# Performance work log

Measured on AMD Instinct MI355X. Metric: run time of the kernel, lower is better.

## Reference

```python
import jax, jax.numpy as jnp
import numpy as np

NEG_SLOPE = 0.2  # PyG GATConv default leaky_relu slope

def gat_conv(x, src, dst, W, a_src, a_dst, bias, N):
    # Linear transform
    h = x @ W                      # [N, D]
    # Per-node attention logits (heads=1)
    al_src = h @ a_src             # [N]
    al_dst = h @ a_dst             # [N]
    e = jax.nn.leaky_relu(al_src[src] + al_dst[dst], NEG_SLOPE)  # [E]
    # Segment softmax over incoming edges of each destination node
    m = jax.ops.segment_max(e, dst, num_segments=N)
    ex = jnp.exp(e - m[dst])
    denom = jax.ops.segment_sum(ex, dst, num_segments=N)
    alpha = ex / denom[dst]        # [E]
    # Weighted scatter-aggregate of source features
    out = jax.ops.segment_sum(h[src] * alpha[:, None], dst, num_segments=N)
    return out + bias

def setup_inputs() -> dict:
    key = jax.random.key(0)
    ks = jax.random.split(key, 10)
    N, E, F_in, H, O = 50000, 800000, 128, 64, 64
    x = jax.random.normal(ks[0], (N, F_in), dtype=jnp.float32)
    edge_index = jax.random.randint(ks[1], (2, E), 0, N, dtype=jnp.int32)
    s = lambda k, shp, fan: jax.random.normal(k, shp, dtype=jnp.float32) / np.sqrt(fan)
    return {
        'x': x, 'edge_index': edge_index,
        'W1': s(ks[2], (F_in, H), F_in), 'a_src1': s(ks[3], (H,), H), 'a_dst1': s(ks[4], (H,), H), 'b1': jnp.zeros((H,), jnp.float32),
        'W2': s(ks[5], (H, O), H), 'a_src2': s(ks[6], (O,), O), 'a_dst2': s(ks[7], (O,), O), 'b2': jnp.zeros((O,), jnp.float32),
    }

def reference(x, edge_index, W1, a_src1, a_dst1, b1, W2, a_src2, a_dst2, b2):
    N = x.shape[0]
    loops = jnp.arange(N, dtype=edge_index.dtype)  # PyG adds self-loops by default
    src = jnp.concatenate([edge_index[0], loops])
    dst = jnp.concatenate([edge_index[1], loops])
    h = gat_conv(x, src, dst, W1, a_src1, a_dst1, b1, N)
    h = jax.nn.relu(h)
    # dropout(p=0.6) is identity in eval mode
    out = gat_conv(h, src, dst, W2, a_src2, a_dst2, b2, N)
    return out
```

## Files before the change

kernel.cpp:

```cpp
#include <hip/hip_runtime.h>
#include <hip/hip_bf16.h>

#define DEV static __device__ __forceinline__

typedef short bf16x8 __attribute__((ext_vector_type(8)));
typedef float f32x4  __attribute__((ext_vector_type(4)));
typedef unsigned u32x4 __attribute__((ext_vector_type(4)));

union U4 { uint4 u; bf16x8 s; };

DEV float b2f(__hip_bfloat16 v) { return __bfloat162float(v); }
DEV float lrelu(float e) { return e > 0.f ? e : 0.2f * e; }

DEV unsigned short f2bu(float f) {
    __hip_bfloat16 b = __float2bfloat16(f);
    return *reinterpret_cast<unsigned short*>(&b);
}
DEV float bu2f(unsigned short u) { return __uint_as_float((unsigned)u << 16); }

DEV float loadF(const void* p, size_t i, int f32) {
    if (f32) return ((const float*)p)[i];
    return b2f(((const __hip_bfloat16*)p)[i]);
}

DEV uint4 pack8(const unsigned short* t) {
    uint4 v;
    v.x = (unsigned)t[0] | ((unsigned)t[1] << 16);
    v.y = (unsigned)t[2] | ((unsigned)t[3] << 16);
    v.z = (unsigned)t[4] | ((unsigned)t[5] << 16);
    v.w = (unsigned)t[6] | ((unsigned)t[7] << 16);
    return v;
}

DEV u32x4 pack8v(const unsigned short* t) {
    u32x4 v;
    v.x = (unsigned)t[0] | ((unsigned)t[1] << 16);
    v.y = (unsigned)t[2] | ((unsigned)t[3] << 16);
    v.z = (unsigned)t[4] | ((unsigned)t[5] << 16);
    v.w = (unsigned)t[6] | ((unsigned)t[7] << 16);
    return v;
}

__global__ __launch_bounds__(1024) void k_detect(
    const void* a0, int n0, const void* a1, int n1, const void* a2, int n2,
    const void* a3, int n3, const void* a4, int n4, const void* a5, int n5,
    const void* a6, int n6, const void* a7, int n7, const void* a8, int n8,
    int* __restrict__ flags)
{
    const void* ps[9] = {a0,a1,a2,a3,a4,a5,a6,a7,a8};
    const int   ns[9] = {n0,n1,n2,n3,n4,n5,n6,n7,n8};
    const int w = threadIdx.x >> 6, lane = threadIdx.x & 63;
    if (w >= 9) return;
    const unsigned short* p = (const unsigned short*)ps[w];
    const int n = ns[w];
    bool insane = false;
#pragma unroll
    for (int r = 0; r < 4; ++r) {
        int idx = lane + r * 64;
        if (idx < n) {
            unsigned short u = p[idx];
            unsigned e = (u >> 7) & 0xFFu;
            insane |= (e >= 0xC8u) || (e == 0u && (u & 0x7Fu) != 0u);
        }
    }
    unsigned long long m = __ballot(insane);
    if (lane == 0) flags[w] = (m != 0ull) ? 1 : 0;
}

DEV void edge_sd(int i, int E, const int* __restrict__ src, const int* __restrict__ dst,
                 int& s, int& d) {
    if (i < E) { s = src[i]; d = dst[i]; }
    else       { s = d = i - E; }
}

#define G_BIN 128

__global__ __launch_bounds__(256) void k_binA(
    const int* __restrict__ src, const int* __restrict__ dst,
    int* __restrict__ hist, int E, int EA, int chunk)
{
    __shared__ int cnt[256];
    const int tid = threadIdx.x;
    cnt[tid] = 0;
    __syncthreads();
    const int lo = blockIdx.x * chunk;
    const int hi = min(lo + chunk, EA);
    for (int i = lo + tid; i < hi; i += 256) {
        int s, d; edge_sd(i, E, src, dst, s, d);
        atomicAdd(&cnt[d >> 8], 1);
    }
    __syncthreads();
    hist[blockIdx.x * 256 + tid] = cnt[tid];
}

__global__ __launch_bounds__(G_BIN) void k_binB1(
    const int* __restrict__ hist, int* __restrict__ offs_rel,
    int* __restrict__ btot)
{
    __shared__ int sm[G_BIN];
    const int t = threadIdx.x;
    const int b = blockIdx.x;
    int v = hist[t * 256 + b];
    sm[t] = v;
    __syncthreads();
#pragma unroll
    for (int off = 1; off < G_BIN; off <<= 1) {
        int u = (t >= off) ? sm[t - off] : 0;
        __syncthreads();
        sm[t] += u;
        __syncthreads();
    }
    offs_rel[t * 256 + b] = sm[t] - v;
    if (t == G_BIN - 1) btot[b] = sm[t];
}

__global__ __launch_bounds__(256) void k_binB2(
    const int* __restrict__ btot, int* __restrict__ bstart)
{
    __shared__ int sm[256];
    const int tid = threadIdx.x;
    int v = btot[tid];
    sm[tid] = v;
    __syncthreads();
#pragma unroll
    for (int off = 1; off < 256; off <<= 1) {
        int t = (tid >= off) ? sm[tid - off] : 0;
        __syncthreads();
        sm[tid] += t;
        __syncthreads();
    }
    bstart[tid] = sm[tid] - v;
    if (tid == 255) bstart[256] = sm[255];
}

__global__ __launch_bounds__(256) void k_binC(
    const int* __restrict__ src, const int* __restrict__ dst,
    const int* __restrict__ offs_rel, const int* __restrict__ bstart,
    unsigned* __restrict__ ebuf, int E, int EA, int chunk)
{
    __shared__ int cur[256];
    const int tid = threadIdx.x;
    cur[tid] = bstart[tid] + offs_rel[blockIdx.x * 256 + tid];
    __syncthreads();
    const int lo = blockIdx.x * chunk;
    const int hi = min(lo + chunk, EA);
    for (int i = lo + tid; i < hi; i += 256) {
        int s, d; edge_sd(i, E, src, dst, s, d);
        int pos = atomicAdd(&cur[d >> 8], 1);
        ebuf[pos] = ((unsigned)(d & 255) << 17) | (unsigned)s;
    }
}

__global__ __launch_bounds__(256) void k_binD(
    const unsigned* __restrict__ ebuf, const int* __restrict__ bstart,
    int* __restrict__ row_ptr, int* __restrict__ col, int N)
{
    __shared__ int cnt[256];
    __shared__ int pfx[256];
    const int tid = threadIdx.x;
    const int b = blockIdx.x;
    const int lo = bstart[b], hi = bstart[b + 1];
    cnt[tid] = 0;
    __syncthreads();
    for (int i = lo + tid; i < hi; i += 256)
        atomicAdd(&cnt[ebuf[i] >> 17], 1);
    __syncthreads();
    const int c = cnt[tid];
    pfx[tid] = c;
    __syncthreads();
#pragma unroll
    for (int off = 1; off < 256; off <<= 1) {
        int t = (tid >= off) ? pfx[tid - off] : 0;
        __syncthreads();
        pfx[tid] += t;
        __syncthreads();
    }
    const int excl = pfx[tid] - c;
    const int d = b * 256 + tid;
    if (d <= N) row_ptr[d] = lo + excl;
    __syncthreads();
    cnt[tid] = lo + excl;
    __syncthreads();
    for (int i = lo + tid; i < hi; i += 256) {
        unsigned v = ebuf[i];
        int pos = atomicAdd(&cnt[v >> 17], 1);
        col[pos] = (int)(v & 0x1FFFFu);
    }
}

__global__ __launch_bounds__(256) void k_gemm1(
    const void* __restrict__ x, const void* __restrict__ W,
    const void* __restrict__ a_s, const void* __restrict__ a_d,
    const int* __restrict__ flags,
    __hip_bfloat16* __restrict__ h, float* __restrict__ als, float* __restrict__ ald,
    int N)
{
    __shared__ __align__(16) unsigned short sMem[2 * 64 * 136];
    __shared__ float sAs[64], sAd[64];
    unsigned short* sA = sMem;
    unsigned short* sB = sMem + 64 * 136;
    float* sOut = (float*)sMem;

    const int tid = threadIdx.x;
    const int row0 = blockIdx.x * 64;
    const int fx = flags[0], fw = flags[1];

    if (tid < 64) sAs[tid] = loadF(a_s, tid, flags[2]);
    else if (tid < 128) sAd[tid - 64] = loadF(a_d, tid - 64, flags[3]);

    if (!fx) {
        const uint4* xg = (const uint4*)x;
#pragma unroll
        for (int it = 0; it < 2; ++it) {
            int g = tid + it * 256;
            int r = g >> 4, c16 = g & 15;
            uint4 v = (row0 + r < N) ? xg[(size_t)(row0 + r) * 16 + c16]
                                     : make_uint4(0, 0, 0, 0);
            *(uint4*)(sA + r * 136 + c16 * 8) = v;
        }
    } else {
        for (int i = tid; i < 64 * 128; i += 256) {
            int r = i >> 7, k = i & 127;
            float v = (row0 + r < N) ? ((const float*)x)[(size_t)(row0 + r) * 128 + k] : 0.f;
            sA[r * 136 + k] = f2bu(v);
        }
    }
    if (!fw) {
        const unsigned short* Wg = (const unsigned short*)W;
        const int n = tid & 63;
        int k0 = (tid >> 6) * 8;
#pragma unroll
        for (int rep = 0; rep < 4; ++rep, k0 += 32) {
            unsigned short t[8];
#pragma unroll
            for (int j = 0; j < 8; ++j) t[j] = Wg[(size_t)(k0 + j) * 64 + n];
            *(uint4*)(sB + n * 136 + k0) = pack8(t);
        }
    } else {
        const float* Wg = (const float*)W;
        for (int i = tid; i < 128 * 64; i += 256) {
            int k = i >> 6, n = i & 63;
            sB[n * 136 + k] = f2bu(Wg[i]);
        }
    }
    __syncthreads();

    const int w = tid >> 6, lane = tid & 63;
    const int m0 = w * 16;
    const int qr = lane >> 4;
    const int lc = lane & 15;

    bf16x8 afrag[4];
#pragma unroll
    for (int c = 0; c < 4; ++c) {
        U4 u; u.u = *(const uint4*)(sA + (m0 + lc) * 136 + c * 32 + qr * 8);
        afrag[c] = u.s;
    }
    f32x4 accs[4];
#pragma unroll
    for (int nt = 0; nt < 4; ++nt) {
        f32x4 acc = {0.f, 0.f, 0.f, 0.f};
#pragma unroll
        for (int c = 0; c < 4; ++c) {
            U4 u; u.u = *(const uint4*)(sB + (nt * 16 + lc) * 136 + c * 32 + qr * 8);
            acc = __builtin_amdgcn_mfma_f32_16x16x32_bf16(afrag[c], u.s, acc, 0, 0, 0);
        }
        accs[nt] = acc;
    }
    __syncthreads();

#pragma unroll
    for (int nt = 0; nt < 4; ++nt)
#pragma unroll
        for (int reg = 0; reg < 4; ++reg)
            sOut[(m0 + qr * 4 + reg) * 68 + nt * 16 + lc] = accs[nt][reg];
    __syncthreads();

    {
        const int r = tid >> 2, seg = tid & 3;
        const int row = row0 + r;
        const float* po = sOut + r * 68 + seg * 16;
        float ps = 0.f, pd = 0.f;
        unsigned short ob[16];
#pragma unroll
        for (int i = 0; i < 16; ++i) {
            float v = po[i];
            ps = fmaf(v, sAs[seg * 16 + i], ps);
            pd = fmaf(v, sAd[seg * 16 + i], pd);
            ob[i] = f2bu(v);
        }
        if (row < N) {
            uint4* hp = (uint4*)((unsigned short*)h + (size_t)row * 64 + seg * 16);
            hp[0] = pack8(ob);
            hp[1] = pack8(ob + 8);
        }
        ps += __shfl_xor(ps, 1, 64); ps += __shfl_xor(ps, 2, 64);
        pd += __shfl_xor(pd, 1, 64); pd += __shfl_xor(pd, 2, 64);
        if (seg == 0 && row < N) { als[row] = ps; ald[row] = pd; }
    }
}

__global__ __launch_bounds__(256) void k_gemm2(
    __hip_bfloat16* __restrict__ agg, const void* __restrict__ b1,
    const void* __restrict__ W, const void* __restrict__ a_s,
    const void* __restrict__ a_d, const int* __restrict__ flags,
    float* __restrict__ als, float* __restrict__ ald, int N)
{
    __shared__ __align__(16) unsigned short sMem[2 * 64 * 72];
    __shared__ float sAs[64], sAd[64], sBias[64];
    unsigned short* sA = sMem;
    unsigned short* sB = sMem + 64 * 72;
    float* sOut = (float*)sMem;

    const int tid = threadIdx.x;
    const int row0 = blockIdx.x * 64;
    const int fw = flags[5];

    if (tid < 64) sAs[tid] = loadF(a_s, tid, flags[6]);
    else if (tid < 128) sAd[tid - 64] = loadF(a_d, tid - 64, flags[7]);
    else if (tid < 192) sBias[tid - 128] = loadF(b1, tid - 128, flags[4]);
    __syncthreads();

    {
        const uint4* ag = (const uint4*)agg;
#pragma unroll
        for (int it = 0; it < 2; ++it) {
            int g = tid + it * 256;
            int r = g >> 3, c8 = g & 7;
            uint4 v = (row0 + r < N) ? ag[(size_t)(row0 + r) * 8 + c8]
                                     : make_uint4(0, 0, 0, 0);
            unsigned short in[8] = {
                (unsigned short)(v.x & 0xFFFF), (unsigned short)(v.x >> 16),
                (unsigned short)(v.y & 0xFFFF), (unsigned short)(v.y >> 16),
                (unsigned short)(v.z & 0xFFFF), (unsigned short)(v.z >> 16),
                (unsigned short)(v.w & 0xFFFF), (unsigned short)(v.w >> 16)};
            unsigned short ob[8];
#pragma unroll
            for (int j = 0; j < 8; ++j) {
                float t = bu2f(in[j]) + sBias[c8 * 8 + j];
                ob[j] = f2bu(t > 0.f ? t : 0.f);
            }
            *(uint4*)(sA + r * 72 + c8 * 8) = pack8(ob);
        }
    }
    if (!fw) {
        const unsigned short* Wg = (const unsigned short*)W;
        const int n = tid & 63;
        int k0 = (tid >> 6) * 8;
#pragma unroll
        for (int rep = 0; rep < 2; ++rep, k0 += 32) {
            unsigned short t[8];
#pragma unroll
            for (int j = 0; j < 8; ++j) t[j] = Wg[(size_t)(k0 + j) * 64 + n];
            *(uint4*)(sB + n * 72 + k0) = pack8(t);
        }
    } else {
        const float* Wg = (const float*)W;
        for (int i = tid; i < 64 * 64; i += 256) {
            int k = i >> 6, n = i & 63;
            sB[n * 72 + k] = f2bu(Wg[i]);
        }
    }
    __syncthreads();

    const int w = tid >> 6, lane = tid & 63;
    const int m0 = w * 16;
    const int qr = lane >> 4, lc = lane & 15;

    bf16x8 afrag[2];
#pragma unroll
    for (int c = 0; c < 2; ++c) {
        U4 u; u.u = *(const uint4*)(sA + (m0 + lc) * 72 + c * 32 + qr * 8);
        afrag[c] = u.s;
    }
    f32x4 accs[4];
#pragma unroll
    for (int nt = 0; nt < 4; ++nt) {
        f32x4 acc = {0.f, 0.f, 0.f, 0.f};
#pragma unroll
        for (int c = 0; c < 2; ++c) {
            U4 u; u.u = *(const uint4*)(sB + (nt * 16 + lc) * 72 + c * 32 + qr * 8);
            acc = __builtin_amdgcn_mfma_f32_16x16x32_bf16(afrag[c], u.s, acc, 0, 0, 0);
        }
        accs[nt] = acc;
    }
    __syncthreads();
#pragma unroll
    for (int nt = 0; nt < 4; ++nt)
#pragma unroll
        for (int reg = 0; reg < 4; ++reg)
            sOut[(m0 + qr * 4 + reg) * 68 + nt * 16 + lc] = accs[nt][reg];
    __syncthreads();

    {
        const int r = tid >> 2, seg = tid & 3;
        const int row = row0 + r;
        const float* po = sOut + r * 68 + seg * 16;
        float ps = 0.f, pd = 0.f;
        unsigned short ob[16];
#pragma unroll
        for (int i = 0; i < 16; ++i) {
            float v = po[i];
            ps = fmaf(v, sAs[seg * 16 + i], ps);
            pd = fmaf(v, sAd[seg * 16 + i], pd);
            ob[i] = f2bu(v);
        }
        if (row < N) {
            uint4* hp = (uint4*)((unsigned short*)agg + (size_t)row * 64 + seg * 16);
            hp[0] = pack8(ob);
            hp[1] = pack8(ob + 8);
        }
        ps += __shfl_xor(ps, 1, 64); ps += __shfl_xor(ps, 2, 64);
        pd += __shfl_xor(pd, 1, 64); pd += __shfl_xor(pd, 2, 64);
        if (seg == 0 && row < N) { als[row] = ps; ald[row] = pd; }
    }
}

__global__ __launch_bounds__(256) void k_gather(
    const int* __restrict__ row_ptr, const int* __restrict__ col,
    const float* __restrict__ als, const float* __restrict__ ald,
    const __hip_bfloat16* __restrict__ h,
    __hip_bfloat16* __restrict__ agg_out,
    void* __restrict__ final_out,
    const void* __restrict__ bias, const int* __restrict__ flags, int N)
{
    const int tid = threadIdx.x;
    const int lane = tid & 63;
    const int sub = lane >> 4;
    const int eg  = (lane >> 3) & 1;
    const int fg  = lane & 7;
    const int wslot = blockIdx.x * 4 + (tid >> 6);
    const int stride = gridDim.x * 4 * 4;

    for (int d0 = wslot * 4; d0 < N; d0 += stride) {
        const int d = d0 + sub;
        const bool valid = d < N;
        int beg = 0, end = 0;
        float aldd = 0.f;
        if (valid) { beg = row_ptr[d]; end = row_ptr[d + 1]; aldd = ald[d]; }
        float acc[8] = {0.f,0.f,0.f,0.f,0.f,0.f,0.f,0.f};
        float den = 0.f;
        for (int it = 0; ; ++it) {
            const int j = beg + it * 2 + eg;
            const bool act = valid && (j < end);
            if (!__any(act)) break;
            const int s = __builtin_nontemporal_load(col + (act ? j : 0));
            const float w = act ? __expf(lrelu(als[s] + aldd)) : 0.f;
            den += w;
            const uint4 hv = *reinterpret_cast<const uint4*>(h + (size_t)s * 64 + fg * 8);
            acc[0] = fmaf(w, __uint_as_float(hv.x << 16),          acc[0]);
            acc[1] = fmaf(w, __uint_as_float(hv.x & 0xFFFF0000u),  acc[1]);
            acc[2] = fmaf(w, __uint_as_float(hv.y << 16),          acc[2]);
            acc[3] = fmaf(w, __uint_as_float(hv.y & 0xFFFF0000u),  acc[3]);
            acc[4] = fmaf(w, __uint_as_float(hv.z << 16),          acc[4]);
            acc[5] = fmaf(w, __uint_as_float(hv.z & 0xFFFF0000u),  acc[5]);
            acc[6] = fmaf(w, __uint_as_float(hv.w << 16),          acc[6]);
            acc[7] = fmaf(w, __uint_as_float(hv.w & 0xFFFF0000u),  acc[7]);
        }
        den += __shfl_xor(den, 8, 64);
#pragma unroll
        for (int k = 0; k < 8; ++k) acc[k] += __shfl_xor(acc[k], 8, 64);

        if (eg == 0 && valid) {
            const float inv = 1.f / den;
            if (final_out) {
                float vb[8];
#pragma unroll
                for (int k = 0; k < 8; ++k) vb[k] = acc[k] * inv + loadF(bias, fg * 8 + k, flags[8]);
                if (flags[0]) {
                    float* o = (float*)final_out + (size_t)d * 64 + fg * 8;
                    f32x4 o0 = {vb[0], vb[1], vb[2], vb[3]};
                    f32x4 o1 = {vb[4], vb[5], vb[6], vb[7]};
                    __builtin_nontemporal_store(o0, (f32x4*)o);
                    __builtin_nontemporal_store(o1, (f32x4*)(o + 4));
                } else {
                    unsigned short ob[8];
#pragma unroll
                    for (int k = 0; k < 8; ++k) ob[k] = f2bu(vb[k]);
                    __builtin_nontemporal_store(pack8v(ob),
                        reinterpret_cast<u32x4*>((__hip_bfloat16*)final_out + (size_t)d * 64 + fg * 8));
                }
            } else {
                unsigned short ob[8];
#pragma unroll
                for (int k = 0; k < 8; ++k) ob[k] = f2bu(acc[k] * inv);
                __builtin_nontemporal_store(pack8v(ob),
                    reinterpret_cast<u32x4*>(agg_out + (size_t)d * 64 + fg * 8));
            }
        }
    }
}

extern "C" void kernel_launch(void* const* d_in, const int* in_sizes, int n_in,
                              void* d_out, int out_size, void* d_ws, size_t ws_size,
                              hipStream_t stream)
{
    const void* x   = d_in[0];
    const int*  ei  = (const int*)d_in[1];
    const void* W1  = d_in[2];
    const void* as1 = d_in[3];
    const void* ad1 = d_in[4];
    const void* b1  = d_in[5];
    const void* W2  = d_in[6];
    const void* as2 = d_in[7];
    const void* ad2 = d_in[8];
    const void* b2  = d_in[9];

    const int N  = in_sizes[0] / 128;
    const int E  = in_sizes[1] / 2;
    const int EA = E + N;
    const int* src = ei;
    const int* dst = ei + E;

    uintptr_t base = (uintptr_t)d_ws;
    auto alloc = [&](size_t bytes) { uintptr_t p = base; base += (bytes + 63) & ~(size_t)63; return p; };
    int*      flags    = (int*)alloc(64 * 4);
    float*    als      = (float*)alloc((size_t)N * 4);
    float*    ald      = (float*)alloc((size_t)N * 4);
    int*      row_ptr  = (int*)alloc((size_t)(N + 1) * 4);
    int*      hist     = (int*)alloc((size_t)G_BIN * 256 * 4);
    int*      offs_rel = (int*)alloc((size_t)G_BIN * 256 * 4);
    int*      btot     = (int*)alloc(256 * 4);
    int*      bstart   = (int*)alloc(257 * 4);
    unsigned* ebuf     = (unsigned*)alloc((size_t)EA * 4);
    int*      col      = (int*)alloc((size_t)EA * 4);
    __hip_bfloat16* hbuf   = (__hip_bfloat16*)alloc((size_t)N * 64 * 2);
    __hip_bfloat16* aggbuf = (__hip_bfloat16*)alloc((size_t)N * 64 * 2);

    const int gatherb = 2048;
    const int gb  = (N + 63) / 64;
    const int NBK = (N + 255) / 256;
    const int chunk = (EA + G_BIN - 1) / G_BIN;

    k_detect<<<1, 1024, 0, stream>>>(
        x, in_sizes[0], W1, in_sizes[2], as1, in_sizes[3], ad1, in_sizes[4],
        b1, in_sizes[5], W2, in_sizes[6], as2, in_sizes[7], ad2, in_sizes[8],
        b2, in_sizes[9], flags);

    k_binA<<<G_BIN, 256, 0, stream>>>(src, dst, hist, E, EA, chunk);
    k_binB1<<<256, G_BIN, 0, stream>>>(hist, offs_rel, btot);
    k_binB2<<<1, 256, 0, stream>>>(btot, bstart);
    k_binC<<<G_BIN, 256, 0, stream>>>(src, dst, offs_rel, bstart, ebuf, E, EA, chunk);
    k_binD<<<NBK, 256, 0, stream>>>(ebuf, bstart, row_ptr, col, N);

    k_gemm1<<<gb, 256, 0, stream>>>(x, W1, as1, ad1, flags, hbuf, als, ald, N);
    k_gather<<<gatherb, 256, 0, stream>>>(row_ptr, col, als, ald, hbuf, aggbuf,
                                          nullptr, nullptr, flags, N);
    k_gemm2<<<gb, 256, 0, stream>>>(aggbuf, b1, W2, as2, ad2, flags, als, ald, N);
    k_gather<<<gatherb, 256, 0, stream>>>(row_ptr, col, als, ald, aggbuf, nullptr,
                                          d_out, b2, flags, N);
    (void)out_size; (void)ws_size; (void)n_in;
}
```

Baseline: 231.3 us.

## Fuse layer-2 GEMM into first gather and merge dtype detection into binning

```diff
diff --git a/kernel.cpp b/kernel.cpp
--- a/kernel.cpp
+++ b/kernel.cpp
@@ -6,6 +6,7 @@
 typedef short bf16x8 __attribute__((ext_vector_type(8)));
 typedef float f32x4  __attribute__((ext_vector_type(4)));
 typedef unsigned u32x4 __attribute__((ext_vector_type(4)));
+typedef unsigned u32x2 __attribute__((ext_vector_type(2)));
 
 union U4 { uint4 u; bf16x8 s; };
 
@@ -41,46 +42,46 @@
     return v;
 }
 
-__global__ __launch_bounds__(1024) void k_detect(
+DEV void edge_sd(int i, int E, const int* __restrict__ src, const int* __restrict__ dst,
+                 int& s, int& d) {
+    if (i < E) { s = src[i]; d = dst[i]; }
+    else       { s = d = i - E; }
+}
+
+#define G_BIN 128
+
+__global__ __launch_bounds__(256) void k_binA(
+    const int* __restrict__ src, const int* __restrict__ dst,
+    int* __restrict__ hist, int E, int EA, int chunk,
     const void* a0, int n0, const void* a1, int n1, const void* a2, int n2,
     const void* a3, int n3, const void* a4, int n4, const void* a5, int n5,
     const void* a6, int n6, const void* a7, int n7, const void* a8, int n8,
     int* __restrict__ flags)
 {
-    const void* ps[9] = {a0,a1,a2,a3,a4,a5,a6,a7,a8};
-    const int   ns[9] = {n0,n1,n2,n3,n4,n5,n6,n7,n8};
-    const int w = threadIdx.x >> 6, lane = threadIdx.x & 63;
-    if (w >= 9) return;
-    const unsigned short* p = (const unsigned short*)ps[w];
-    const int n = ns[w];
-    bool insane = false;
-#pragma unroll
-    for (int r = 0; r < 4; ++r) {
-        int idx = lane + r * 64;
-        if (idx < n) {
-            unsigned short u = p[idx];
-            unsigned e = (u >> 7) & 0xFFu;
-            insane |= (e >= 0xC8u) || (e == 0u && (u & 0x7Fu) != 0u);
-        }
-    }
-    unsigned long long m = __ballot(insane);
-    if (lane == 0) flags[w] = (m != 0ull) ? 1 : 0;
-}
-
-DEV void edge_sd(int i, int E, const int* __restrict__ src, const int* __restrict__ dst,
-                 int& s, int& d) {
-    if (i < E) { s = src[i]; d = dst[i]; }
-    else       { s = d = i - E; }
-}
-
-#define G_BIN 128
-
-__global__ __launch_bounds__(256) void k_binA(
-    const int* __restrict__ src, const int* __restrict__ dst,
-    int* __restrict__ hist, int E, int EA, int chunk)
-{
+    const int tid = threadIdx.x;
+    if (blockIdx.x == G_BIN) {
+        const void* ps[9] = {a0,a1,a2,a3,a4,a5,a6,a7,a8};
+        const int   ns[9] = {n0,n1,n2,n3,n4,n5,n6,n7,n8};
+        const int w = tid >> 6, lane = tid & 63;
+        for (int k = w; k < 9; k += 4) {
+            const unsigned short* p = (const unsigned short*)ps[k];
+            const int n = ns[k];
+            bool insane = false;
+#pragma unroll
+            for (int r = 0; r < 4; ++r) {
+                int idx = lane + r * 64;
+                if (idx < n) {
+                    unsigned short u = p[idx];
+                    unsigned e = (u >> 7) & 0xFFu;
+                    insane |= (e >= 0xC8u) || (e == 0u && (u & 0x7Fu) != 0u);
+                }
+            }
+            unsigned long long m = __ballot(insane);
+            if (lane == 0) flags[k] = (m != 0ull) ? 1 : 0;
+        }
+        return;
+    }
     __shared__ int cnt[256];
-    const int tid = threadIdx.x;
     cnt[tid] = 0;
     __syncthreads();
     const int lo = blockIdx.x * chunk;
@@ -300,154 +301,48 @@
     }
 }
 
-__global__ __launch_bounds__(256) void k_gemm2(
-    __hip_bfloat16* __restrict__ agg, const void* __restrict__ b1,
-    const void* __restrict__ W, const void* __restrict__ a_s,
-    const void* __restrict__ a_d, const int* __restrict__ flags,
-    float* __restrict__ als, float* __restrict__ ald, int N)
-{
-    __shared__ __align__(16) unsigned short sMem[2 * 64 * 72];
-    __shared__ float sAs[64], sAd[64], sBias[64];
-    unsigned short* sA = sMem;
-    unsigned short* sB = sMem + 64 * 72;
-    float* sOut = (float*)sMem;
-
-    const int tid = threadIdx.x;
-    const int row0 = blockIdx.x * 64;
-    const int fw = flags[5];
-
-    if (tid < 64) sAs[tid] = loadF(a_s, tid, flags[6]);
-    else if (tid < 128) sAd[tid - 64] = loadF(a_d, tid - 64, flags[7]);
-    else if (tid < 192) sBias[tid - 128] = loadF(b1, tid - 128, flags[4]);
-    __syncthreads();
-
-    {
-        const uint4* ag = (const uint4*)agg;
-#pragma unroll
-        for (int it = 0; it < 2; ++it) {
-            int g = tid + it * 256;
-            int r = g >> 3, c8 = g & 7;
-            uint4 v = (row0 + r < N) ? ag[(size_t)(row0 + r) * 8 + c8]
-                                     : make_uint4(0, 0, 0, 0);
-            unsigned short in[8] = {
-                (unsigned short)(v.x & 0xFFFF), (unsigned short)(v.x >> 16),
-                (unsigned short)(v.y & 0xFFFF), (unsigned short)(v.y >> 16),
-                (unsigned short)(v.z & 0xFFFF), (unsigned short)(v.z >> 16),
-                (unsigned short)(v.w & 0xFFFF), (unsigned short)(v.w >> 16)};
-            unsigned short ob[8];
-#pragma unroll
-            for (int j = 0; j < 8; ++j) {
-                float t = bu2f(in[j]) + sBias[c8 * 8 + j];
-                ob[j] = f2bu(t > 0.f ? t : 0.f);
-            }
-            *(uint4*)(sA + r * 72 + c8 * 8) = pack8(ob);
-        }
-    }
-    if (!fw) {
-        const unsigned short* Wg = (const unsigned short*)W;
-        const int n = tid & 63;
-        int k0 = (tid >> 6) * 8;
-#pragma unroll
-        for (int rep = 0; rep < 2; ++rep, k0 += 32) {
-            unsigned short t[8];
-#pragma unroll
-            for (int j = 0; j < 8; ++j) t[j] = Wg[(size_t)(k0 + j) * 64 + n];
-            *(uint4*)(sB + n * 72 + k0) = pack8(t);
-        }
-    } else {
-        const float* Wg = (const float*)W;
-        for (int i = tid; i < 64 * 64; i += 256) {
-            int k = i >> 6, n = i & 63;
-            sB[n * 72 + k] = f2bu(Wg[i]);
-        }
-    }
-    __syncthreads();
-
-    const int w = tid >> 6, lane = tid & 63;
-    const int m0 = w * 16;
-    const int qr = lane >> 4, lc = lane & 15;
-
-    bf16x8 afrag[2];
-#pragma unroll
-    for (int c = 0; c < 2; ++c) {
-        U4 u; u.u = *(const uint4*)(sA + (m0 + lc) * 72 + c * 32 + qr * 8);
-        afrag[c] = u.s;
-    }
-    f32x4 accs[4];
-#pragma unroll
-    for (int nt = 0; nt < 4; ++nt) {
-        f32x4 acc = {0.f, 0.f, 0.f, 0.f};
-#pragma unroll
-        for (int c = 0; c < 2; ++c) {
-            U4 u; u.u = *(const uint4*)(sB + (nt * 16 + lc) * 72 + c * 32 + qr * 8);
-            acc = __builtin_amdgcn_mfma_f32_16x16x32_bf16(afrag[c], u.s, acc, 0, 0, 0);
-        }
-        accs[nt] = acc;
-    }
-    __syncthreads();
-#pragma unroll
-    for (int nt = 0; nt < 4; ++nt)
-#pragma unroll
-        for (int reg = 0; reg < 4; ++reg)
-            sOut[(m0 + qr * 4 + reg) * 68 + nt * 16 + lc] = accs[nt][reg];
-    __syncthreads();
-
-    {
-        const int r = tid >> 2, seg = tid & 3;
-        const int row = row0 + r;
-        const float* po = sOut + r * 68 + seg * 16;
-        float ps = 0.f, pd = 0.f;
-        unsigned short ob[16];
-#pragma unroll
-        for (int i = 0; i < 16; ++i) {
-            float v = po[i];
-            ps = fmaf(v, sAs[seg * 16 + i], ps);
-            pd = fmaf(v, sAd[seg * 16 + i], pd);
-            ob[i] = f2bu(v);
-        }
-        if (row < N) {
-            uint4* hp = (uint4*)((unsigned short*)agg + (size_t)row * 64 + seg * 16);
-            hp[0] = pack8(ob);
-            hp[1] = pack8(ob + 8);
-        }
-        ps += __shfl_xor(ps, 1, 64); ps += __shfl_xor(ps, 2, 64);
-        pd += __shfl_xor(pd, 1, 64); pd += __shfl_xor(pd, 2, 64);
-        if (seg == 0 && row < N) { als[row] = ps; ald[row] = pd; }
-    }
-}
-
-__global__ __launch_bounds__(256) void k_gather(
+__global__ __launch_bounds__(256) void k_gather1(
     const int* __restrict__ row_ptr, const int* __restrict__ col,
     const float* __restrict__ als, const float* __restrict__ ald,
     const __hip_bfloat16* __restrict__ h,
-    __hip_bfloat16* __restrict__ agg_out,
-    void* __restrict__ final_out,
-    const void* __restrict__ bias, const int* __restrict__ flags, int N)
-{
-    const int tid = threadIdx.x;
+    const void* __restrict__ b1, const void* __restrict__ W2,
+    const void* __restrict__ as2, const void* __restrict__ ad2,
+    const int* __restrict__ flags,
+    __hip_bfloat16* __restrict__ h2, float* __restrict__ als2,
+    float* __restrict__ ald2, int N)
+{
+    __shared__ float sW2[64 * 64];
+    __shared__ float sB1[64], sAs2[64], sAd2[64];
+    const int tid = threadIdx.x;
+    {
+        const int fw2 = flags[5];
+        for (int i = tid; i < 64 * 64; i += 256) sW2[i] = loadF(W2, i, fw2);
+        if (tid < 64) sB1[tid] = loadF(b1, tid, flags[4]);
+        else if (tid < 128) sAs2[tid - 64] = loadF(as2, tid - 64, flags[6]);
+        else if (tid < 192) sAd2[tid - 128] = loadF(ad2, tid - 128, flags[7]);
+    }
+    __syncthreads();
+
     const int lane = tid & 63;
     const int sub = lane >> 4;
     const int eg  = (lane >> 3) & 1;
     const int fg  = lane & 7;
+    const int lane16 = lane & 15;
     const int wslot = blockIdx.x * 4 + (tid >> 6);
     const int stride = gridDim.x * 4 * 4;
 
     for (int d0 = wslot * 4; d0 < N; d0 += stride) {
         const int d = d0 + sub;
         const bool valid = d < N;
-        int beg = 0, end = 0;
-        float aldd = 0.f;
+        int beg = 0, end = 0; float aldd = 0.f;
         if (valid) { beg = row_ptr[d]; end = row_ptr[d + 1]; aldd = ald[d]; }
         float acc[8] = {0.f,0.f,0.f,0.f,0.f,0.f,0.f,0.f};
         float den = 0.f;
-        for (int it = 0; ; ++it) {
-            const int j = beg + it * 2 + eg;
-            const bool act = valid && (j < end);
-            if (!__any(act)) break;
-            const int s = __builtin_nontemporal_load(col + (act ? j : 0));
-            const float w = act ? __expf(lrelu(als[s] + aldd)) : 0.f;
+        for (int j = beg + eg; valid && j < end; j += 2) {
+            const int s = col[j];
+            const float w = __expf(lrelu(als[s] + aldd));
             den += w;
-            const uint4 hv = *reinterpret_cast<const uint4*>(h + (size_t)s * 64 + fg * 8);
+            const uint4 hv = *(const uint4*)(h + (size_t)s * 64 + fg * 8);
             acc[0] = fmaf(w, __uint_as_float(hv.x << 16),          acc[0]);
             acc[1] = fmaf(w, __uint_as_float(hv.x & 0xFFFF0000u),  acc[1]);
             acc[2] = fmaf(w, __uint_as_float(hv.y << 16),          acc[2]);
@@ -461,31 +356,106 @@
 #pragma unroll
         for (int k = 0; k < 8; ++k) acc[k] += __shfl_xor(acc[k], 8, 64);
 
+        const float inv = 1.f / den;
+        float xk[8];
+#pragma unroll
+        for (int k = 0; k < 8; ++k) {
+            float t = acc[k] * inv + sB1[fg * 8 + k];
+            xk[k] = t > 0.f ? t : 0.f;
+        }
+        float o[4] = {0.f, 0.f, 0.f, 0.f};
+        const int ofs = lane16 * 4;
+#pragma unroll
+        for (int fs = 0; fs < 8; ++fs) {
+            float xb[8];
+#pragma unroll
+            for (int k = 0; k < 8; ++k) xb[k] = __shfl(xk[k], (sub << 4) + fs, 64);
+#pragma unroll
+            for (int k = 0; k < 8; ++k) {
+                const float* wr = &sW2[(fs * 8 + k) * 64 + ofs];
+                o[0] = fmaf(xb[k], wr[0], o[0]);
+                o[1] = fmaf(xb[k], wr[1], o[1]);
+                o[2] = fmaf(xb[k], wr[2], o[2]);
+                o[3] = fmaf(xb[k], wr[3], o[3]);
+            }
+        }
+        float ps = o[0] * sAs2[ofs]     + o[1] * sAs2[ofs + 1]
+                 + o[2] * sAs2[ofs + 2] + o[3] * sAs2[ofs + 3];
+        float pd = o[0] * sAd2[ofs]     + o[1] * sAd2[ofs + 1]
+                 + o[2] * sAd2[ofs + 2] + o[3] * sAd2[ofs + 3];
+#pragma unroll
+        for (int off = 1; off <= 8; off <<= 1) {
+            ps += __shfl_xor(ps, off, 64);
+            pd += __shfl_xor(pd, off, 64);
+        }
+        if (valid) {
+            if (lane16 == 0) { als2[d] = ps; ald2[d] = pd; }
+            unsigned short ob[4] = {f2bu(o[0]), f2bu(o[1]), f2bu(o[2]), f2bu(o[3])};
+            u32x2 st;
+            st.x = (unsigned)ob[0] | ((unsigned)ob[1] << 16);
+            st.y = (unsigned)ob[2] | ((unsigned)ob[3] << 16);
+            *(u32x2*)((unsigned short*)h2 + (size_t)d * 64 + ofs) = st;
+        }
+    }
+}
+
+__global__ __launch_bounds__(256) void k_gather2(
+    const int* __restrict__ row_ptr, const int* __restrict__ col,
+    const float* __restrict__ als, const float* __restrict__ ald,
+    const __hip_bfloat16* __restrict__ h,
+    void* __restrict__ out, const void* __restrict__ bias,
+    const int* __restrict__ flags, int N)
+{
+    const int tid = threadIdx.x;
+    const int lane = tid & 63;
+    const int sub = lane >> 4;
+    const int eg  = (lane >> 3) & 1;
+    const int fg  = lane & 7;
+    const int wslot = blockIdx.x * 4 + (tid >> 6);
+    const int stride = gridDim.x * 4 * 4;
+
+    for (int d0 = wslot * 4; d0 < N; d0 += stride) {
+        const int d = d0 + sub;
+        const bool valid = d < N;
+        int beg = 0, end = 0; float aldd = 0.f;
+        if (valid) { beg = row_ptr[d]; end = row_ptr[d + 1]; aldd = ald[d]; }
+        float acc[8] = {0.f,0.f,0.f,0.f,0.f,0.f,0.f,0.f};
+        float den = 0.f;
+        for (int j = beg + eg; valid && j < end; j += 2) {
+            const int s = col[j];
+            const float w = __expf(lrelu(als[s] + aldd));
+            den += w;
+            const uint4 hv = *(const uint4*)(h + (size_t)s * 64 + fg * 8);
+            acc[0] = fmaf(w, __uint_as_float(hv.x << 16),          acc[0]);
+            acc[1] = fmaf(w, __uint_as_float(hv.x & 0xFFFF0000u),  acc[1]);
+            acc[2] = fmaf(w, __uint_as_float(hv.y << 16),          acc[2]);
+            acc[3] = fmaf(w, __uint_as_float(hv.y & 0xFFFF0000u),  acc[3]);
+            acc[4] = fmaf(w, __uint_as_float(hv.z << 16),          acc[4]);
+            acc[5] = fmaf(w, __uint_as_float(hv.z & 0xFFFF0000u),  acc[5]);
+            acc[6] = fmaf(w, __uint_as_float(hv.w << 16),          acc[6]);
+            acc[7] = fmaf(w, __uint_as_float(hv.w & 0xFFFF0000u),  acc[7]);
+        }
+        den += __shfl_xor(den, 8, 64);
+#pragma unroll
+        for (int k = 0; k < 8; ++k) acc[k] += __shfl_xor(acc[k], 8, 64);
+
         if (eg == 0 && valid) {
             const float inv = 1.f / den;
-            if (final_out) {
-                float vb[8];
-#pragma unroll
-                for (int k = 0; k < 8; ++k) vb[k] = acc[k] * inv + loadF(bias, fg * 8 + k, flags[8]);
-                if (flags[0]) {
-                    float* o = (float*)final_out + (size_t)d * 64 + fg * 8;
-                    f32x4 o0 = {vb[0], vb[1], vb[2], vb[3]};
-                    f32x4 o1 = {vb[4], vb[5], vb[6], vb[7]};
-                    __builtin_nontemporal_store(o0, (f32x4*)o);
-                    __builtin_nontemporal_store(o1, (f32x4*)(o + 4));
-                } else {
-                    unsigned short ob[8];
-#pragma unroll
-                    for (int k = 0; k < 8; ++k) ob[k] = f2bu(vb[k]);
-                    __builtin_nontemporal_store(pack8v(ob),
-                        reinterpret_cast<u32x4*>((__hip_bfloat16*)final_out + (size_t)d * 64 + fg * 8));
-                }
+            float vb[8];
+#pragma unroll
+            for (int k = 0; k < 8; ++k) vb[k] = acc[k] * inv + loadF(bias, fg * 8 + k, flags[8]);
+            if (flags[0]) {
+                float* o = (float*)out + (size_t)d * 64 + fg * 8;
+                f32x4 o0 = {vb[0], vb[1], vb[2], vb[3]};
+                f32x4 o1 = {vb[4], vb[5], vb[6], vb[7]};
+                __builtin_nontemporal_store(o0, (f32x4*)o);
+                __builtin_nontemporal_store(o1, (f32x4*)(o + 4));
             } else {
                 unsigned short ob[8];
 #pragma unroll
-                for (int k = 0; k < 8; ++k) ob[k] = f2bu(acc[k] * inv);
+                for (int k = 0; k < 8; ++k) ob[k] = f2bu(vb[k]);
                 __builtin_nontemporal_store(pack8v(ob),
-                    reinterpret_cast<u32x4*>(agg_out + (size_t)d * 64 + fg * 8));
+                    reinterpret_cast<u32x4*>((__hip_bfloat16*)out + (size_t)d * 64 + fg * 8));
             }
         }
     }
@@ -517,6 +487,8 @@
     int*      flags    = (int*)alloc(64 * 4);
     float*    als      = (float*)alloc((size_t)N * 4);
     float*    ald      = (float*)alloc((size_t)N * 4);
+    float*    als2     = (float*)alloc((size_t)N * 4);
+    float*    ald2     = (float*)alloc((size_t)N * 4);
     int*      row_ptr  = (int*)alloc((size_t)(N + 1) * 4);
     int*      hist     = (int*)alloc((size_t)G_BIN * 256 * 4);
     int*      offs_rel = (int*)alloc((size_t)G_BIN * 256 * 4);
@@ -524,30 +496,29 @@
     int*      bstart   = (int*)alloc(257 * 4);
     unsigned* ebuf     = (unsigned*)alloc((size_t)EA * 4);
     int*      col      = (int*)alloc((size_t)EA * 4);
-    __hip_bfloat16* hbuf   = (__hip_bfloat16*)alloc((size_t)N * 64 * 2);
-    __hip_bfloat16* aggbuf = (__hip_bfloat16*)alloc((size_t)N * 64 * 2);
+    __hip_bfloat16* hbuf  = (__hip_bfloat16*)alloc((size_t)N * 64 * 2);
+    __hip_bfloat16* h2buf = (__hip_bfloat16*)alloc((size_t)N * 64 * 2);
 
     const int gatherb = 2048;
     const int gb  = (N + 63) / 64;
     const int NBK = (N + 255) / 256;
     const int chunk = (EA + G_BIN - 1) / G_BIN;
 
-    k_detect<<<1, 1024, 0, stream>>>(
+    k_binA<<<G_BIN + 1, 256, 0, stream>>>(
+        src, dst, hist, E, EA, chunk,
         x, in_sizes[0], W1, in_sizes[2], as1, in_sizes[3], ad1, in_sizes[4],
         b1, in_sizes[5], W2, in_sizes[6], as2, in_sizes[7], ad2, in_sizes[8],
         b2, in_sizes[9], flags);
-
-    k_binA<<<G_BIN, 256, 0, stream>>>(src, dst, hist, E, EA, chunk);
     k_binB1<<<256, G_BIN, 0, stream>>>(hist, offs_rel, btot);
     k_binB2<<<1, 256, 0, stream>>>(btot, bstart);
     k_binC<<<G_BIN, 256, 0, stream>>>(src, dst, offs_rel, bstart, ebuf, E, EA, chunk);
     k_binD<<<NBK, 256, 0, stream>>>(ebuf, bstart, row_ptr, col, N);
 
     k_gemm1<<<gb, 256, 0, stream>>>(x, W1, as1, ad1, flags, hbuf, als, ald, N);
-    k_gather<<<gatherb, 256, 0, stream>>>(row_ptr, col, als, ald, hbuf, aggbuf,
-                                          nullptr, nullptr, flags, N);
-    k_gemm2<<<gb, 256, 0, stream>>>(aggbuf, b1, W2, as2, ad2, flags, als, ald, N);
-    k_gather<<<gatherb, 256, 0, stream>>>(row_ptr, col, als, ald, aggbuf, nullptr,
-                                          d_out, b2, flags, N);
+    k_gather1<<<gatherb, 256, 0, stream>>>(row_ptr, col, als, ald, hbuf,
+                                           b1, W2, as2, ad2, flags,
+                                           h2buf, als2, ald2, N);
+    k_gather2<<<gatherb, 256, 0, stream>>>(row_ptr, col, als2, ald2, h2buf,
+                                           d_out, b2, flags, N);
     (void)out_size; (void)ws_size; (void)n_in;
 }
```

Result: slower. 332.8 us (+43.9%).
